# Kernel optimization log

Measured on AMD Instinct MI355X. Metric: run time of the kernel, lower is better.

The kernel has to match this reference:

```python
import jax, jax.numpy as jnp
import numpy as np

T, H = 1024, 2048          # tokens, hidden_size
E, K = 8, 4                # num_experts, top_k
I_E = 1408                 # moe_intermediate_size
I_S = 5632                 # shared_expert_intermediate_size


def setup_inputs() -> dict:
    key = jax.random.key(0)
    ks = jax.random.split(key, 7)
    s = 0.02
    return {
        "hidden_states": jax.random.normal(ks[0], (T, H), dtype=jnp.float32),
        "w_gate": jax.random.normal(ks[1], (H, E), dtype=jnp.float32) * s,
        "w_shared_gate": jax.random.normal(ks[2], (H, 1), dtype=jnp.float32) * s,
        "w_shared_gu": jax.random.normal(ks[3], (H, 2 * I_S), dtype=jnp.float32) * s,
        "w_shared_down": jax.random.normal(ks[4], (I_S, H), dtype=jnp.float32) * s,
        "w_exp_gu": jax.random.normal(ks[5], (E, H, 2 * I_E), dtype=jnp.float32) * s,
        "w_exp_down": jax.random.normal(ks[6], (E, I_E, H), dtype=jnp.float32) * s,
    }


def _silu_and_mul(gu):
    g, u = jnp.split(gu, 2, axis=-1)
    return jax.nn.silu(g) * u


def reference(hidden_states, w_gate, w_shared_gate, w_shared_gu, w_shared_down,
              w_exp_gu, w_exp_down):
    x = hidden_states  # [T, H]

    # ---- router: softmax -> top_k (norm_topk_prob=False, no renormalize) ----
    router_logits = x @ w_gate                       # [T, E]
    probs = jax.nn.softmax(router_logits, axis=-1)
    topw, topi = jax.lax.top_k(probs, K)             # [T, K] each
    # per-token combine weights over experts: [T, E]
    comb = jnp.sum(jax.nn.one_hot(topi, E, dtype=probs.dtype) * topw[..., None], axis=1)

    # ---- fused experts (dense-per-expert reference for grouped GEMM) ----
    gu = jnp.einsum('th,ehf->etf', x, w_exp_gu)      # [E, T, 2*I_E]
    act = _silu_and_mul(gu)                          # [E, T, I_E]
    out_e = jnp.einsum('etf,efh->eth', act, w_exp_down)  # [E, T, H]
    fused_out = jnp.einsum('eth,te->th', out_e, comb)    # [T, H]

    # ---- shared expert with sigmoid gate ----
    s_act = _silu_and_mul(x @ w_shared_gu)           # [T, I_S]
    shared_out = s_act @ w_shared_down               # [T, H]
    shared_out = jax.nn.sigmoid(x @ w_shared_gate) * shared_out

    return shared_out + fused_out
```

## Files before the change

### kernel.cpp

```cpp
#include <hip/hip_runtime.h>
#include <hip/hip_bf16.h>
#include <stdint.h>

#define T_TOK 1024
#define H_DIM 2048
#define NEXP 8
#define IED 1408
#define ISD 5632

typedef __attribute__((ext_vector_type(8))) short s16x8;
typedef __attribute__((ext_vector_type(8))) unsigned short u16x8;
typedef __attribute__((ext_vector_type(4))) float f32x4;

__device__ __forceinline__ unsigned short f2bf(float f) {
  union { float f; unsigned u; } v; v.f = f;
  unsigned r = v.u + 0x7FFFu + ((v.u >> 16) & 1u);
  return (unsigned short)(r >> 16);
}

__device__ __forceinline__ void gload16(const void* g, void* l) {
  __builtin_amdgcn_global_load_lds(
      (const __attribute__((address_space(1))) unsigned int*)g,
      (__attribute__((address_space(3))) unsigned int*)l, 16, 0, 0);
}

extern "C" __global__ void __launch_bounds__(256) k_cvt(
    const float* __restrict__ x, unsigned short* __restrict__ xb) {
  int i = (blockIdx.x * 256 + threadIdx.x) * 4;
  float4 v = *(const float4*)(x + i);
  ushort4 o;
  o.x = f2bf(v.x); o.y = f2bf(v.y); o.z = f2bf(v.z); o.w = f2bf(v.w);
  *(ushort4*)(xb + i) = o;
}

extern "C" __global__ void __launch_bounds__(256) k_router(
    const float* __restrict__ x, const float* __restrict__ wg,
    const float* __restrict__ wsg, int* __restrict__ counts,
    int* __restrict__ tlist, float* __restrict__ wlist,
    float* __restrict__ gate_sig) {
  const int lane = threadIdx.x & 63;
  const int t = blockIdx.x * 4 + (threadIdx.x >> 6);
  const float* xr = x + (size_t)t * H_DIM;
  float acc[8];
#pragma unroll
  for (int e = 0; e < 8; e++) acc[e] = 0.f;
  float sg = 0.f;
  for (int h = lane; h < H_DIM; h += 64) {
    float xv = xr[h];
    float4 w0 = *(const float4*)(wg + h * 8);
    float4 w1 = *(const float4*)(wg + h * 8 + 4);
    acc[0] += xv * w0.x; acc[1] += xv * w0.y; acc[2] += xv * w0.z; acc[3] += xv * w0.w;
    acc[4] += xv * w1.x; acc[5] += xv * w1.y; acc[6] += xv * w1.z; acc[7] += xv * w1.w;
    sg += xv * wsg[h];
  }
#pragma unroll
  for (int d = 32; d >= 1; d >>= 1) {
#pragma unroll
    for (int e = 0; e < 8; e++) acc[e] += __shfl_xor(acc[e], d, 64);
    sg += __shfl_xor(sg, d, 64);
  }
  if (lane == 0) {
    float m = acc[0];
#pragma unroll
    for (int e = 1; e < 8; e++) m = fmaxf(m, acc[e]);
    float p[8], s = 0.f;
#pragma unroll
    for (int e = 0; e < 8; e++) { p[e] = __expf(acc[e] - m); s += p[e]; }
    float inv = 1.f / s;
    bool used[8];
#pragma unroll
    for (int e = 0; e < 8; e++) used[e] = false;
    for (int j = 0; j < 4; j++) {
      int be = 0; float bv = -1e30f;
#pragma unroll
      for (int e = 0; e < 8; e++)
        if (!used[e] && acc[e] > bv) { bv = acc[e]; be = e; }
      used[be] = true;
      int slot = atomicAdd(counts + be, 1);
      tlist[be * T_TOK + slot] = t;
      wlist[be * T_TOK + slot] = p[be] * inv;
    }
    gate_sig[t] = 1.f / (1.f + __expf(-sg));
  }
}

#define ISSUE_A(kk, OFFS)                                                 \
  do {                                                                    \
    _Pragma("unroll") for (int q = 0; q < 4; q++)                         \
        gload16(asrc[q] + (kk), adst[q] + (OFFS));                        \
  } while (0)

#define ISSUE_B(kk)                                                       \
  do {                                                                    \
    _Pragma("unroll") for (int i = 0; i < 8; i++) {                       \
      size_t ko = (size_t)((kk) + bkset + i) * (size_t)ldb;               \
      RBg[i] = *(const float2*)(B0 + ko + bn);                            \
      RBu[i] = *(const float2*)(B1 + ko + bn);                            \
    }                                                                     \
  } while (0)

#define CVTB(OFFS)                                                        \
  do {                                                                    \
    _Pragma("unroll") for (int jj = 0; jj < 2; jj++) {                    \
      u16x8 pg, pu;                                                       \
      _Pragma("unroll") for (int i = 0; i < 8; i++) {                     \
        pg[i] = f2bf(jj ? RBg[i].y : RBg[i].x);                           \
        pu[i] = f2bf(jj ? RBu[i].y : RBu[i].x);                           \
      }                                                                   \
      *(u16x8*)(bwr[0][jj] + (OFFS)) = pg;                                \
      *(u16x8*)(bwr[1][jj] + (OFFS)) = pu;                                \
    }                                                                     \
  } while (0)

#define COMPUTE(OFFS)                                                     \
  do {                                                                    \
    const unsigned short* ab = a_lds + (OFFS);                            \
    const unsigned short* bb = b_lds + (OFFS);                            \
    __builtin_amdgcn_s_setprio(1);                                        \
    _Pragma("unroll") for (int ks = 0; ks < 2; ks++) {                    \
      int kc = ks * 4 + (lane >> 4);                                      \
      s16x8 afr[4];                                                       \
      _Pragma("unroll") for (int m = 0; m < 4; m++) {                     \
        int r = wm * 64 + m * 16 + (lane & 15);                           \
        afr[m] = *(const s16x8*)&ab[r * 64 + ((kc ^ (r & 7)) * 8)];       \
      }                                                                   \
      _Pragma("unroll") for (int nf = 0; nf < 4; nf++) {                  \
        int rb_;                                                          \
        if constexpr (MODE < 2) rb_ = wn * 32 + (nf & 1) * 16 + (nf >> 1) * 64; \
        else rb_ = wn * 64 + nf * 16;                                     \
        rb_ += (lane & 15);                                               \
        s16x8 bfr = *(const s16x8*)&bb[rb_ * 64 + ((kc ^ (rb_ & 7)) * 8)]; \
        _Pragma("unroll") for (int m = 0; m < 4; m++)                     \
            acc[m][nf] = __builtin_amdgcn_mfma_f32_16x16x32_bf16(         \
                afr[m], bfr, acc[m][nf], 0, 0, 0);                        \
      }                                                                   \
    }                                                                     \
    __builtin_amdgcn_s_setprio(0);                                        \
  } while (0)

template <int MODE>
__global__ void __launch_bounds__(256, 2) k_mm(
    const unsigned short* __restrict__ Abase, const float* __restrict__ Bbase,
    unsigned short* __restrict__ actout, float* __restrict__ out,
    const int* __restrict__ counts, const int* __restrict__ tlist,
    const float* __restrict__ wlist, const float* __restrict__ gate_sig) {
  const int tid = threadIdx.x;
  const int lane = tid & 63;
  const int wid = tid >> 6;
  const int wm = wid >> 1, wn = wid & 1;

  constexpr int P = (MODE == 0) ? 88 : (MODE == 1) ? 176 : (MODE == 2) ? 64 : 128;
  const int b = blockIdx.x;
  const int xcd = b & 7;
  const int j = b >> 3;
  const int panel = xcd * (P >> 3) + (j >> 3);
  const int mtile = j & 7;
  int ntile = 0, z = 0, e = 0;
  if constexpr (MODE == 0) { ntile = panel; }
  else if constexpr (MODE == 1) { e = panel & 7; ntile = panel >> 3; }
  else if constexpr (MODE == 2) { ntile = panel >> 2; z = panel & 3; }
  else { e = panel & 7; ntile = panel >> 3; }

  int count = T_TOK, kbeg = 0, kend = 0, lda = 0, ldb = 0, IK = 0;
  const unsigned short* A = Abase;
  const float* B0 = nullptr; const float* B1 = nullptr;
  const int* tl = nullptr; const float* wl = nullptr;

  if constexpr (MODE == 0) {
    lda = H_DIM; kend = H_DIM; ldb = 2 * ISD; IK = ISD;
    B0 = Bbase + ntile * 64; B1 = Bbase + ISD + ntile * 64;
  } else if constexpr (MODE == 1) {
    count = counts[e];
    if (mtile * 128 >= count) return;
    lda = H_DIM; kend = H_DIM; ldb = 2 * IED; IK = IED;
    const float* Bw = Bbase + (size_t)e * H_DIM * (2 * IED);
    B0 = Bw + ntile * 64; B1 = Bw + IED + ntile * 64;
    tl = tlist + e * T_TOK; wl = wlist + e * T_TOK;
    actout += (size_t)e * T_TOK * IED;
  } else if constexpr (MODE == 2) {
    lda = ISD; kbeg = z * 1408; kend = kbeg + 1408; ldb = H_DIM; IK = H_DIM;
    B0 = Bbase + ntile * 128; B1 = Bbase + ntile * 128 + 64;
  } else {
    count = counts[e];
    if (mtile * 128 >= count) return;
    lda = IED; kend = IED; ldb = H_DIM; IK = H_DIM;
    B0 = Bbase + (size_t)e * IED * H_DIM + ntile * 128;
    B1 = B0 + 64;
    A = Abase + (size_t)e * T_TOK * IED;
    tl = tlist + e * T_TOK;
  }

  __shared__ unsigned short a_lds[2 * 8192];
  __shared__ unsigned short b_lds[2 * 8192];

  const unsigned short* asrc[4];
  unsigned short* adst[4];
#pragma unroll
  for (int q = 0; q < 4; q++) {
    int row = wid * 32 + q * 8 + (lane >> 3);
    int rowg = mtile * 128 + row;
    int arow = rowg;
    if constexpr (MODE == 1) arow = tl[rowg];
    int kc = (lane & 7) ^ ((lane >> 3) & 7);
    asrc[q] = A + (size_t)arow * lda + kc * 8;
    adst[q] = &a_lds[(wid * 4 + q) * 512];
  }

  const int bn = (tid & 31) * 2;
  const int bkset = ((tid >> 5) & 7) * 8;
  const int bkc = (tid >> 5) & 7;
  unsigned short* bwr[2][2];
#pragma unroll
  for (int h = 0; h < 2; h++)
#pragma unroll
    for (int jj = 0; jj < 2; jj++) {
      int r = h * 64 + bn + jj;
      bwr[h][jj] = &b_lds[r * 64 + ((bkc ^ (r & 7)) * 8)];
    }

  const f32x4 fzero = {0.f, 0.f, 0.f, 0.f};
  f32x4 acc[4][4];
#pragma unroll
  for (int m = 0; m < 4; m++)
#pragma unroll
    for (int n = 0; n < 4; n++) acc[m][n] = fzero;

  const int nt = (kend - kbeg) >> 6;
  float2 RBg[8], RBu[8];

  ISSUE_B(kbeg);
  ISSUE_A(kbeg, 0);
  CVTB(0);
  ISSUE_B(kbeg + 64);
  __builtin_amdgcn_sched_barrier(0);
  asm volatile("s_waitcnt vmcnt(16)" ::: "memory");
  asm volatile("s_waitcnt lgkmcnt(0)" ::: "memory");
  __builtin_amdgcn_s_barrier();
  __builtin_amdgcn_sched_barrier(0);

  for (int u = 0; u < nt; ++u) {
    const int cur = (u & 1) * 8192;
    const int nxt = cur ^ 8192;
    const int k0 = kbeg + u * 64;
    const bool haveN1 = (u + 1 < nt);
    const bool haveN2 = (u + 2 < nt);
    if (haveN1) {
      ISSUE_A(k0 + 64, nxt);
      CVTB(nxt);
      if (haveN2) ISSUE_B(k0 + 128);
    }
    COMPUTE(cur);
    if (haveN1) {
      __builtin_amdgcn_sched_barrier(0);
      if (haveN2)
        asm volatile("s_waitcnt vmcnt(16)" ::: "memory");
      else
        asm volatile("s_waitcnt vmcnt(0)" ::: "memory");
      asm volatile("s_waitcnt lgkmcnt(0)" ::: "memory");
      __builtin_amdgcn_s_barrier();
      __builtin_amdgcn_sched_barrier(0);
    }
  }

  if constexpr (MODE < 2) {
#pragma unroll
    for (int m = 0; m < 4; m++) {
#pragma unroll
      for (int i = 0; i < 4; i++) {
        int rowslot = mtile * 128 + wm * 64 + m * 16 + (lane >> 4) * 4 + i;
        float rsc = 1.f;
        if constexpr (MODE == 1) rsc = wl[rowslot];
#pragma unroll
        for (int p = 0; p < 2; p++) {
          float g = acc[m][p][i];
          float u2 = acc[m][p + 2][i];
          float sv = g / (1.f + __expf(-g)) * u2 * rsc;
          int col = ntile * 64 + wn * 32 + p * 16 + (lane & 15);
          actout[(size_t)rowslot * IK + col] = f2bf(sv);
        }
      }
    }
  } else {
#pragma unroll
    for (int m = 0; m < 4; m++) {
#pragma unroll
      for (int i = 0; i < 4; i++) {
        int rowslot = mtile * 128 + wm * 64 + m * 16 + (lane >> 4) * 4 + i;
        int token = rowslot;
        if constexpr (MODE == 3) token = tl[rowslot];
        float sc = 1.f;
        if constexpr (MODE == 2) sc = gate_sig[token];
        float* orow = out + (size_t)token * H_DIM + ntile * 128 + wn * 64 + (lane & 15);
#pragma unroll
        for (int nf = 0; nf < 4; nf++)
          atomicAdd(orow + nf * 16, acc[m][nf][i] * sc);
      }
    }
  }
}

extern "C" void kernel_launch(void* const* d_in, const int* in_sizes, int n_in,
                              void* d_out, int out_size, void* d_ws, size_t ws_size,
                              hipStream_t stream) {
  (void)in_sizes; (void)n_in; (void)out_size; (void)ws_size;
  const float* x    = (const float*)d_in[0];
  const float* wg   = (const float*)d_in[1];
  const float* wsg  = (const float*)d_in[2];
  const float* wsgu = (const float*)d_in[3];
  const float* wsd  = (const float*)d_in[4];
  const float* wegu = (const float*)d_in[5];
  const float* wed  = (const float*)d_in[6];
  float* out = (float*)d_out;

  char* ws = (char*)d_ws;
  unsigned short* xb   = (unsigned short*)ws;
  unsigned short* acts = (unsigned short*)(ws + (4u << 20));
  unsigned short* acte = (unsigned short*)(ws + (4u << 20) + 11534336u);
  char* ctrl = ws + (4u << 20) + 11534336u + 23068672u;
  int* counts    = (int*)ctrl;
  int* tlist     = (int*)(ctrl + 256);
  float* wlist   = (float*)(ctrl + 256 + 32768);
  float* gate_sig = (float*)(ctrl + 256 + 65536);

  hipMemsetAsync(d_out, 0, (size_t)T_TOK * H_DIM * 4, stream);
  hipMemsetAsync(ctrl, 0, 256 + 65536, stream);

  k_cvt<<<dim3(2048), dim3(256), 0, stream>>>(x, xb);
  k_router<<<dim3(256), dim3(256), 0, stream>>>(x, wg, wsg, counts, tlist, wlist, gate_sig);
  k_mm<0><<<dim3(704), dim3(256), 0, stream>>>(xb, wsgu, acts, out, counts, tlist, wlist, gate_sig);
  k_mm<1><<<dim3(1408), dim3(256), 0, stream>>>(xb, wegu, acte, out, counts, tlist, wlist, gate_sig);
  k_mm<2><<<dim3(512), dim3(256), 0, stream>>>(acts, wsd, nullptr, out, counts, tlist, wlist, gate_sig);
  k_mm<3><<<dim3(1024), dim3(256), 0, stream>>>(acte, wed, nullptr, out, counts, tlist, wlist, gate_sig);
}
```

Baseline: 513.0 us.

## Merge shared and expert GEMMs into combined launches with BK=32 tiles

Folds the bf16 conversion of x into the router kernel. Merges the shared-expert and routed-expert GEMMs into a single launch per stage (gate/up, then down), cutting six launches to three. Halves the K tile from 64 to 32 with a new 4-way LDS swizzle, which halves LDS use and raises the occupancy hint from 2 to 4 blocks per CU. The cost is twice as many K iterations and barriers, and branch-dependent setup inside the merged kernels.

```diff
diff --git a/kernel.cpp b/kernel.cpp
--- a/kernel.cpp
+++ b/kernel.cpp
@@ -12,6 +12,8 @@
 typedef __attribute__((ext_vector_type(8))) unsigned short u16x8;
 typedef __attribute__((ext_vector_type(4))) float f32x4;
 
+#define SWZ(r) (((r) ^ ((r) >> 2)) & 3)
+
 __device__ __forceinline__ unsigned short f2bf(float f) {
   union { float f; unsigned u; } v; v.f = f;
   unsigned r = v.u + 0x7FFFu + ((v.u >> 16) & 1u);
@@ -24,22 +26,23 @@
       (__attribute__((address_space(3))) unsigned int*)l, 16, 0, 0);
 }
 
-extern "C" __global__ void __launch_bounds__(256) k_cvt(
-    const float* __restrict__ x, unsigned short* __restrict__ xb) {
-  int i = (blockIdx.x * 256 + threadIdx.x) * 4;
-  float4 v = *(const float4*)(x + i);
-  ushort4 o;
-  o.x = f2bf(v.x); o.y = f2bf(v.y); o.z = f2bf(v.z); o.w = f2bf(v.w);
-  *(ushort4*)(xb + i) = o;
-}
-
 extern "C" __global__ void __launch_bounds__(256) k_router(
     const float* __restrict__ x, const float* __restrict__ wg,
-    const float* __restrict__ wsg, int* __restrict__ counts,
-    int* __restrict__ tlist, float* __restrict__ wlist,
-    float* __restrict__ gate_sig) {
-  const int lane = threadIdx.x & 63;
-  const int t = blockIdx.x * 4 + (threadIdx.x >> 6);
+    const float* __restrict__ wsg, unsigned short* __restrict__ xb,
+    int* __restrict__ counts, int* __restrict__ tlist,
+    float* __restrict__ wlist, float* __restrict__ gate_sig) {
+  const int tid = threadIdx.x;
+  const int bb = blockIdx.x;
+#pragma unroll
+  for (int it = 0; it < 8; it++) {
+    int i = bb * 8192 + it * 1024 + tid * 4;
+    float4 v = *(const float4*)(x + i);
+    ushort4 o;
+    o.x = f2bf(v.x); o.y = f2bf(v.y); o.z = f2bf(v.z); o.w = f2bf(v.w);
+    *(ushort4*)(xb + i) = o;
+  }
+  const int lane = tid & 63;
+  const int t = bb * 4 + (tid >> 6);
   const float* xr = x + (size_t)t * H_DIM;
   float acc[8];
 #pragma unroll
@@ -86,50 +89,45 @@
 
 #define ISSUE_A(kk, OFFS)                                                 \
   do {                                                                    \
-    _Pragma("unroll") for (int q = 0; q < 4; q++)                         \
+    _Pragma("unroll") for (int q = 0; q < 2; q++)                         \
         gload16(asrc[q] + (kk), adst[q] + (OFFS));                        \
+    __builtin_amdgcn_sched_barrier(0);                                    \
   } while (0)
 
 #define ISSUE_B(kk)                                                       \
   do {                                                                    \
-    _Pragma("unroll") for (int i = 0; i < 8; i++) {                       \
-      size_t ko = (size_t)((kk) + bkset + i) * (size_t)ldb;               \
-      RBg[i] = *(const float2*)(B0 + ko + bn);                            \
-      RBu[i] = *(const float2*)(B1 + ko + bn);                            \
-    }                                                                     \
+    _Pragma("unroll") for (int i = 0; i < 8; i++)                         \
+        RB[i] = *(const float2*)(Bh + (size_t)((kk) + bks + i) * (size_t)ldb + bn); \
   } while (0)
 
 #define CVTB(OFFS)                                                        \
   do {                                                                    \
     _Pragma("unroll") for (int jj = 0; jj < 2; jj++) {                    \
-      u16x8 pg, pu;                                                       \
-      _Pragma("unroll") for (int i = 0; i < 8; i++) {                     \
-        pg[i] = f2bf(jj ? RBg[i].y : RBg[i].x);                           \
-        pu[i] = f2bf(jj ? RBu[i].y : RBu[i].x);                           \
-      }                                                                   \
-      *(u16x8*)(bwr[0][jj] + (OFFS)) = pg;                                \
-      *(u16x8*)(bwr[1][jj] + (OFFS)) = pu;                                \
+      u16x8 pk;                                                           \
+      _Pragma("unroll") for (int i = 0; i < 8; i++)                       \
+          pk[i] = f2bf(jj ? RB[i].y : RB[i].x);                           \
+      *(u16x8*)(bwr[jj] + (OFFS)) = pk;                                   \
     }                                                                     \
   } while (0)
 
 #define COMPUTE(OFFS)                                                     \
   do {                                                                    \
     const unsigned short* ab = a_lds + (OFFS);                            \
-    const unsigned short* bb = b_lds + (OFFS);                            \
+    const unsigned short* bb2 = b_lds + (OFFS);                           \
     __builtin_amdgcn_s_setprio(1);                                        \
-    _Pragma("unroll") for (int ks = 0; ks < 2; ks++) {                    \
-      int kc = ks * 4 + (lane >> 4);                                      \
+    {                                                                     \
+      const int kc = lane >> 4;                                           \
       s16x8 afr[4];                                                       \
       _Pragma("unroll") for (int m = 0; m < 4; m++) {                     \
         int r = wm * 64 + m * 16 + (lane & 15);                           \
-        afr[m] = *(const s16x8*)&ab[r * 64 + ((kc ^ (r & 7)) * 8)];       \
+        afr[m] = *(const s16x8*)&ab[r * 32 + ((kc ^ SWZ(r)) * 8)];        \
       }                                                                   \
       _Pragma("unroll") for (int nf = 0; nf < 4; nf++) {                  \
         int rb_;                                                          \
-        if constexpr (MODE < 2) rb_ = wn * 32 + (nf & 1) * 16 + (nf >> 1) * 64; \
-        else rb_ = wn * 64 + nf * 16;                                     \
+        if constexpr (DOWN) rb_ = wn * 64 + nf * 16;                      \
+        else rb_ = wn * 32 + (nf & 1) * 16 + (nf >> 1) * 64;              \
         rb_ += (lane & 15);                                               \
-        s16x8 bfr = *(const s16x8*)&bb[rb_ * 64 + ((kc ^ (rb_ & 7)) * 8)]; \
+        s16x8 bfr = *(const s16x8*)&bb2[rb_ * 32 + ((kc ^ SWZ(rb_)) * 8)]; \
         _Pragma("unroll") for (int m = 0; m < 4; m++)                     \
             acc[m][nf] = __builtin_amdgcn_mfma_f32_16x16x32_bf16(         \
                 afr[m], bfr, acc[m][nf], 0, 0, 0);                        \
@@ -138,10 +136,12 @@
     __builtin_amdgcn_s_setprio(0);                                        \
   } while (0)
 
-template <int MODE>
-__global__ void __launch_bounds__(256, 2) k_mm(
-    const unsigned short* __restrict__ Abase, const float* __restrict__ Bbase,
-    unsigned short* __restrict__ actout, float* __restrict__ out,
+template <int DOWN>
+__global__ void __launch_bounds__(256, 4) k_mm(
+    const unsigned short* __restrict__ A_sh, const unsigned short* __restrict__ A_ex,
+    const float* __restrict__ B_sh, const float* __restrict__ B_ex,
+    unsigned short* __restrict__ act_sh, unsigned short* __restrict__ act_ex,
+    float* __restrict__ out,
     const int* __restrict__ counts, const int* __restrict__ tlist,
     const float* __restrict__ wlist, const float* __restrict__ gate_sig) {
   const int tid = threadIdx.x;
@@ -149,74 +149,85 @@
   const int wid = tid >> 6;
   const int wm = wid >> 1, wn = wid & 1;
 
-  constexpr int P = (MODE == 0) ? 88 : (MODE == 1) ? 176 : (MODE == 2) ? 64 : 128;
-  const int b = blockIdx.x;
+  constexpr int SHBLK = DOWN ? 512 : 704;
+  const int b0 = blockIdx.x;
+  const bool ex = b0 >= SHBLK;
+  const int b = ex ? b0 - SHBLK : b0;
   const int xcd = b & 7;
   const int j = b >> 3;
-  const int panel = xcd * (P >> 3) + (j >> 3);
   const int mtile = j & 7;
-  int ntile = 0, z = 0, e = 0;
-  if constexpr (MODE == 0) { ntile = panel; }
-  else if constexpr (MODE == 1) { e = panel & 7; ntile = panel >> 3; }
-  else if constexpr (MODE == 2) { ntile = panel >> 2; z = panel & 3; }
-  else { e = panel & 7; ntile = panel >> 3; }
-
-  int count = T_TOK, kbeg = 0, kend = 0, lda = 0, ldb = 0, IK = 0;
-  const unsigned short* A = Abase;
-  const float* B0 = nullptr; const float* B1 = nullptr;
-  const int* tl = nullptr; const float* wl = nullptr;
-
-  if constexpr (MODE == 0) {
-    lda = H_DIM; kend = H_DIM; ldb = 2 * ISD; IK = ISD;
-    B0 = Bbase + ntile * 64; B1 = Bbase + ISD + ntile * 64;
-  } else if constexpr (MODE == 1) {
-    count = counts[e];
-    if (mtile * 128 >= count) return;
-    lda = H_DIM; kend = H_DIM; ldb = 2 * IED; IK = IED;
-    const float* Bw = Bbase + (size_t)e * H_DIM * (2 * IED);
-    B0 = Bw + ntile * 64; B1 = Bw + IED + ntile * 64;
-    tl = tlist + e * T_TOK; wl = wlist + e * T_TOK;
-    actout += (size_t)e * T_TOK * IED;
-  } else if constexpr (MODE == 2) {
-    lda = ISD; kbeg = z * 1408; kend = kbeg + 1408; ldb = H_DIM; IK = H_DIM;
-    B0 = Bbase + ntile * 128; B1 = Bbase + ntile * 128 + 64;
+  int e = 0, ntile = 0, z = 0;
+  if constexpr (!DOWN) {
+    if (!ex) ntile = xcd * 11 + (j >> 3);
+    else { int p = xcd * 22 + (j >> 3); e = p & 7; ntile = p >> 3; }
   } else {
-    count = counts[e];
-    if (mtile * 128 >= count) return;
-    lda = IED; kend = IED; ldb = H_DIM; IK = H_DIM;
-    B0 = Bbase + (size_t)e * IED * H_DIM + ntile * 128;
-    B1 = B0 + 64;
-    A = Abase + (size_t)e * T_TOK * IED;
-    tl = tlist + e * T_TOK;
-  }
-
-  __shared__ unsigned short a_lds[2 * 8192];
-  __shared__ unsigned short b_lds[2 * 8192];
-
-  const unsigned short* asrc[4];
-  unsigned short* adst[4];
-#pragma unroll
-  for (int q = 0; q < 4; q++) {
-    int row = wid * 32 + q * 8 + (lane >> 3);
+    if (!ex) { int p = xcd * 8 + (j >> 3); ntile = p >> 2; z = p & 3; }
+    else { int p = xcd * 16 + (j >> 3); e = p & 7; ntile = p >> 3; }
+  }
+
+  int lda, ldb, IK = 0, kbeg = 0, count = T_TOK;
+  const unsigned short* A;
+  const float* B0; const float* B1;
+  const int* tlA = nullptr;
+  const int* tlO = nullptr;
+  const float* wl = nullptr;
+  unsigned short* actout = nullptr;
+
+  if constexpr (!DOWN) {
+    lda = H_DIM;
+    if (!ex) {
+      ldb = 2 * ISD; IK = ISD; A = A_sh; actout = act_sh;
+      B0 = B_sh + ntile * 64; B1 = B_sh + ISD + ntile * 64;
+    } else {
+      count = counts[e];
+      if (mtile * 128 >= count) return;
+      ldb = 2 * IED; IK = IED; A = A_sh;
+      const float* Bw = B_ex + (size_t)e * H_DIM * (2 * IED);
+      B0 = Bw + ntile * 64; B1 = Bw + IED + ntile * 64;
+      tlA = tlist + e * T_TOK; wl = wlist + e * T_TOK;
+      actout = act_ex + (size_t)e * T_TOK * IED;
+    }
+  } else {
+    ldb = H_DIM;
+    if (!ex) {
+      lda = ISD; kbeg = z * 1408; A = A_sh;
+      B0 = B_sh + ntile * 128; B1 = B0 + 64;
+    } else {
+      count = counts[e];
+      if (mtile * 128 >= count) return;
+      lda = IED; A = A_ex + (size_t)e * T_TOK * IED;
+      B0 = B_ex + (size_t)e * IED * H_DIM + ntile * 128; B1 = B0 + 64;
+      tlO = tlist + e * T_TOK;
+    }
+  }
+  const int nt = DOWN ? 44 : 64;
+
+  __shared__ unsigned short a_lds[2 * 4096];
+  __shared__ unsigned short b_lds[2 * 4096];
+
+  const unsigned short* asrc[2];
+  unsigned short* adst[2];
+#pragma unroll
+  for (int q = 0; q < 2; q++) {
+    int row = wid * 32 + q * 16 + (lane >> 2);
     int rowg = mtile * 128 + row;
     int arow = rowg;
-    if constexpr (MODE == 1) arow = tl[rowg];
-    int kc = (lane & 7) ^ ((lane >> 3) & 7);
-    asrc[q] = A + (size_t)arow * lda + kc * 8;
-    adst[q] = &a_lds[(wid * 4 + q) * 512];
-  }
-
+    if (tlA) arow = tlA[rowg];
+    asrc[q] = A + (size_t)arow * lda + (((lane & 3) ^ SWZ(row)) * 8);
+    adst[q] = &a_lds[(wid * 32 + q * 16) * 32];
+  }
+
+  const int half = tid >> 7;
   const int bn = (tid & 31) * 2;
-  const int bkset = ((tid >> 5) & 7) * 8;
-  const int bkc = (tid >> 5) & 7;
-  unsigned short* bwr[2][2];
-#pragma unroll
-  for (int h = 0; h < 2; h++)
-#pragma unroll
-    for (int jj = 0; jj < 2; jj++) {
-      int r = h * 64 + bn + jj;
-      bwr[h][jj] = &b_lds[r * 64 + ((bkc ^ (r & 7)) * 8)];
-    }
+  const int kg = (tid >> 5) & 3;
+  const int bks = kg * 8;
+  const float* Bh = half ? B1 : B0;
+  unsigned short* bwr[2];
+#pragma unroll
+  for (int jj = 0; jj < 2; jj++) {
+    int r = half * 64 + bn + jj;
+    bwr[jj] = &b_lds[r * 32 + ((kg ^ SWZ(r)) * 8)];
+  }
 
   const f32x4 fzero = {0.f, 0.f, 0.f, 0.f};
   f32x4 acc[4][4];
@@ -225,35 +236,34 @@
 #pragma unroll
     for (int n = 0; n < 4; n++) acc[m][n] = fzero;
 
-  const int nt = (kend - kbeg) >> 6;
-  float2 RBg[8], RBu[8];
+  float2 RB[8];
 
   ISSUE_B(kbeg);
   ISSUE_A(kbeg, 0);
   CVTB(0);
-  ISSUE_B(kbeg + 64);
+  ISSUE_B(kbeg + 32);
   __builtin_amdgcn_sched_barrier(0);
-  asm volatile("s_waitcnt vmcnt(16)" ::: "memory");
+  asm volatile("s_waitcnt vmcnt(8)" ::: "memory");
   asm volatile("s_waitcnt lgkmcnt(0)" ::: "memory");
   __builtin_amdgcn_s_barrier();
   __builtin_amdgcn_sched_barrier(0);
 
   for (int u = 0; u < nt; ++u) {
-    const int cur = (u & 1) * 8192;
-    const int nxt = cur ^ 8192;
-    const int k0 = kbeg + u * 64;
+    const int cur = (u & 1) * 4096;
+    const int nxt = cur ^ 4096;
+    const int k0 = kbeg + u * 32;
     const bool haveN1 = (u + 1 < nt);
     const bool haveN2 = (u + 2 < nt);
     if (haveN1) {
-      ISSUE_A(k0 + 64, nxt);
+      ISSUE_A(k0 + 32, nxt);
       CVTB(nxt);
-      if (haveN2) ISSUE_B(k0 + 128);
+      if (haveN2) ISSUE_B(k0 + 64);
     }
     COMPUTE(cur);
     if (haveN1) {
       __builtin_amdgcn_sched_barrier(0);
       if (haveN2)
-        asm volatile("s_waitcnt vmcnt(16)" ::: "memory");
+        asm volatile("s_waitcnt vmcnt(8)" ::: "memory");
       else
         asm volatile("s_waitcnt vmcnt(0)" ::: "memory");
       asm volatile("s_waitcnt lgkmcnt(0)" ::: "memory");
@@ -262,14 +272,14 @@
     }
   }
 
-  if constexpr (MODE < 2) {
+  if constexpr (!DOWN) {
 #pragma unroll
     for (int m = 0; m < 4; m++) {
 #pragma unroll
       for (int i = 0; i < 4; i++) {
         int rowslot = mtile * 128 + wm * 64 + m * 16 + (lane >> 4) * 4 + i;
         float rsc = 1.f;
-        if constexpr (MODE == 1) rsc = wl[rowslot];
+        if (wl) rsc = wl[rowslot];
 #pragma unroll
         for (int p = 0; p < 2; p++) {
           float g = acc[m][p][i];
@@ -287,9 +297,8 @@
       for (int i = 0; i < 4; i++) {
         int rowslot = mtile * 128 + wm * 64 + m * 16 + (lane >> 4) * 4 + i;
         int token = rowslot;
-        if constexpr (MODE == 3) token = tl[rowslot];
-        float sc = 1.f;
-        if constexpr (MODE == 2) sc = gate_sig[token];
+        if (tlO) token = tlO[rowslot];
+        float sc = ex ? 1.f : gate_sig[token];
         float* orow = out + (size_t)token * H_DIM + ntile * 128 + wn * 64 + (lane & 15);
 #pragma unroll
         for (int nf = 0; nf < 4; nf++)
@@ -325,10 +334,9 @@
   hipMemsetAsync(d_out, 0, (size_t)T_TOK * H_DIM * 4, stream);
   hipMemsetAsync(ctrl, 0, 256 + 65536, stream);
 
-  k_cvt<<<dim3(2048), dim3(256), 0, stream>>>(x, xb);
-  k_router<<<dim3(256), dim3(256), 0, stream>>>(x, wg, wsg, counts, tlist, wlist, gate_sig);
-  k_mm<0><<<dim3(704), dim3(256), 0, stream>>>(xb, wsgu, acts, out, counts, tlist, wlist, gate_sig);
-  k_mm<1><<<dim3(1408), dim3(256), 0, stream>>>(xb, wegu, acte, out, counts, tlist, wlist, gate_sig);
-  k_mm<2><<<dim3(512), dim3(256), 0, stream>>>(acts, wsd, nullptr, out, counts, tlist, wlist, gate_sig);
-  k_mm<3><<<dim3(1024), dim3(256), 0, stream>>>(acte, wed, nullptr, out, counts, tlist, wlist, gate_sig);
-}
+  k_router<<<dim3(256), dim3(256), 0, stream>>>(x, wg, wsg, xb, counts, tlist, wlist, gate_sig);
+  k_mm<0><<<dim3(2112), dim3(256), 0, stream>>>(xb, xb, wsgu, wegu, acts, acte, nullptr,
+                                                counts, tlist, wlist, gate_sig);
+  k_mm<1><<<dim3(1536), dim3(256), 0, stream>>>(acts, acte, wsd, wed, nullptr, nullptr, out,
+                                                counts, tlist, wlist, gate_sig);
+}
```

New measurement: 467.8 us. -8.8%, faster.
